# Optimization experiments

Measured on AMD Instinct MI355X. Metric: run time of the kernel, lower is better.

The kernel has to match this reference:

```python
import jax, jax.numpy as jnp
import numpy as np

N_NODES = 100000
N_EDGES = 1600000
D_FEAT = 64
LATENT = 64
N_CLASSES = 16
NEG_SLOPE = 0.01  # flax nn.leaky_relu default negative_slope


def setup_inputs() -> dict:
    key = jax.random.key(0)
    ks = jax.random.split(key, 5)
    nodes = jax.random.normal(ks[0], (N_NODES, D_FEAT), dtype=jnp.float32)
    senders = jax.random.randint(ks[1], (N_EDGES,), 0, N_NODES)
    receivers = jax.random.randint(ks[2], (N_EDGES,), 0, N_NODES)
    # learned params (flax Dense: y = x @ kernel + bias)
    W0 = jax.random.normal(ks[3], (D_FEAT, LATENT), dtype=jnp.float32) / jnp.sqrt(D_FEAT)
    b0 = jnp.zeros((LATENT,), jnp.float32)
    W1 = jax.random.normal(ks[4], (LATENT, N_CLASSES), dtype=jnp.float32) / jnp.sqrt(LATENT)
    b1 = jnp.zeros((N_CLASSES,), jnp.float32)
    return {"nodes": nodes, "senders": senders, "receivers": receivers,
            "W0": W0, "b0": b0, "W1": W1, "b1": b1}


def _gcn_forward(nodes, W0, b0, W1, b1, senders, receivers):
    n = nodes.shape[0]
    ones = jnp.ones_like(senders, dtype=nodes.dtype)
    deg_s = jax.ops.segment_sum(ones, senders, n)    # out-degree of each node as sender
    deg_r = jax.ops.segment_sum(ones, receivers, n)  # in-degree of each node as receiver

    # Layer 1: GraphConvolution(Dense(latent), symmetric_normalization=True)
    h = nodes @ W0 + b0                                                  # [N, latent]
    h = h * jax.lax.rsqrt(jnp.maximum(deg_s, 1.0))[:, None]
    h = jax.ops.segment_sum(h[senders], receivers, n)                    # gather-scatter over edges
    h = h * jax.lax.rsqrt(jnp.maximum(deg_r, 1.0))[:, None]
    h = jnp.where(h >= 0, h, NEG_SLOPE * h)                              # leaky_relu

    # Layer 2: GraphConvolution(Dense(classes)+sigmoid, symmetric_normalization=False)
    z = jax.nn.sigmoid(h @ W1 + b1)                                      # [N, classes]
    out = jax.ops.segment_sum(z[senders], receivers, n)                  # unnormalized aggregation
    return out


def reference(nodes, senders, receivers, W0, b0, W1, b1):
    return _gcn_forward(nodes, W0, b0, W1, b1, senders, receivers)
```

## Files before the change

kernel.cpp:

```cpp
#include <hip/hip_runtime.h>
#include <hip/hip_bf16.h>

#define N_NODES 100000
#define N_EDGES 1600000
#define D 64
#define C 16
#define NEG_SLOPE 0.01f
#define MCAP 64

typedef unsigned int uint32;
typedef unsigned short ushort16;

__device__ __forceinline__ float bf2f(uint32 u) {
    return __uint_as_float(u << 16);
}
__device__ __forceinline__ ushort16 f2bf(float f) {
    __hip_bfloat16 b = __float2bfloat16(f);
    return *reinterpret_cast<ushort16*>(&b);
}

__global__ __launch_bounds__(256) void kA(
        const int* __restrict__ senders, const int* __restrict__ receivers,
        const float* __restrict__ nodes, const float* __restrict__ W0,
        const float* __restrict__ b0,
        int* __restrict__ cnt_s, int* __restrict__ cnt_r,
        int* __restrict__ bucket, ushort16* __restrict__ h) {
    int bid = blockIdx.x;
    if (bid % 5 == 0) {
        int e = (bid / 5) * 256 + threadIdx.x;
        if (e < N_EDGES) {
            int s = senders[e];
            int r = receivers[e];
            atomicAdd(&cnt_s[s], 1);
            int slot = atomicAdd(&cnt_r[r], 1);
            if (slot < MCAP) bucket[r * MCAP + slot] = s;
        }
    } else {
        int gbid = bid - bid / 5 - 1;
        int node = gbid * 4 + (threadIdx.x >> 6);
        int f = threadIdx.x & 63;
        const float* __restrict__ row = nodes + (size_t)node * D;
        float acc = b0[f];
#pragma unroll
        for (int k = 0; k < D; ++k)
            acc = fmaf(row[k], W0[k * D + f], acc);
        h[(size_t)node * D + f] = f2bf(acc);
    }
}

__global__ __launch_bounds__(256) void kB(
        const int* __restrict__ cnt_s, const int* __restrict__ cnt_r,
        const int* __restrict__ bucket, const ushort16* __restrict__ h,
        const float* __restrict__ W1, const float* __restrict__ b1,
        ushort16* __restrict__ z) {
    __shared__ float sm[4][64];
    int wid = threadIdx.x >> 6, lane = threadIdx.x & 63;
    int node = blockIdx.x * 4 + wid;
    int deg = cnt_r[node];
    if (deg > MCAP) deg = MCAP;
    const int* __restrict__ row = bucket + node * MCAP;

    int my = 0; float rq = 0.f;
    if (lane < deg) {
        my = row[lane];
        int ds = cnt_s[my];
        rq = rsqrtf((float)(ds > 1 ? ds : 1));
    }
    int half = lane >> 5, hl = lane & 31;
    float a0 = 0.f, a1 = 0.f;
    for (int k2 = 0; 2 * k2 < deg; ++k2) {
        int ei = 2 * k2 + half;
        int src = __shfl(my, ei, 64);
        float rs = __shfl(rq, ei, 64);
        uint32 w = *(const uint32*)(h + (size_t)src * D + hl * 2);
        if (ei < deg) {
            a0 = fmaf(rs, bf2f(w & 0xffffu), a0);
            a1 = fmaf(rs, bf2f(w >> 16), a1);
        }
    }
    a0 += __shfl_down(a0, 32, 64);
    a1 += __shfl_down(a1, 32, 64);
    if (half == 0) {
        float rr = rsqrtf((float)(deg > 1 ? deg : 1));
        float v0 = a0 * rr; v0 = (v0 >= 0.f) ? v0 : NEG_SLOPE * v0;
        float v1 = a1 * rr; v1 = (v1 >= 0.f) ? v1 : NEG_SLOPE * v1;
        sm[wid][2 * hl] = v0;
        sm[wid][2 * hl + 1] = v1;
    }
    __syncthreads();

    int c = lane & 15, q = lane >> 4;
    float p = 0.f;
#pragma unroll
    for (int i = 0; i < 16; ++i)
        p = fmaf(sm[wid][q * 16 + i], W1[(q * 16 + i) * C + c], p);
    p += __shfl_xor(p, 16, 64);
    p += __shfl_xor(p, 32, 64);
    if (lane < 16) {
        float zc = 1.f / (1.f + expf(-(p + b1[c])));
        z[(size_t)node * C + c] = f2bf(zc);
    }
}

__global__ __launch_bounds__(256) void kC(
        const int* __restrict__ cnt_r, const int* __restrict__ bucket,
        const ushort16* __restrict__ z, float* __restrict__ out) {
    int idx = blockIdx.x * 256 + threadIdx.x;
    int node = idx >> 6;
    int lane = threadIdx.x & 63;
    int g = lane >> 3, p = lane & 7;
    int deg = cnt_r[node];
    if (deg > MCAP) deg = MCAP;
    const int* __restrict__ row = bucket + node * MCAP;

    int my = (lane < deg) ? row[lane] : 0;
    float a0 = 0.f, a1 = 0.f;
    for (int k8 = 0; 8 * k8 < deg; ++k8) {
        int ei = 8 * k8 + g;
        int src = __shfl(my, ei, 64);
        uint32 w = *(const uint32*)(z + (size_t)src * C + p * 2);
        float f0 = bf2f(w & 0xffffu);
        float f1 = bf2f(w >> 16);
        if (ei < deg) { a0 += f0; a1 += f1; }
    }
    a0 += __shfl_xor(a0, 8, 64);  a1 += __shfl_xor(a1, 8, 64);
    a0 += __shfl_xor(a0, 16, 64); a1 += __shfl_xor(a1, 16, 64);
    a0 += __shfl_xor(a0, 32, 64); a1 += __shfl_xor(a1, 32, 64);
    if (lane < 8) {
        float2 o; o.x = a0; o.y = a1;
        *(float2*)(out + (size_t)node * C + p * 2) = o;
    }
}

extern "C" void kernel_launch(void* const* d_in, const int* in_sizes, int n_in,
                              void* d_out, int out_size, void* d_ws, size_t ws_size,
                              hipStream_t stream) {
    const float* nodes     = (const float*)d_in[0];
    const int*   senders   = (const int*)d_in[1];
    const int*   receivers = (const int*)d_in[2];
    const float* W0        = (const float*)d_in[3];
    const float* b0        = (const float*)d_in[4];
    const float* W1        = (const float*)d_in[5];
    const float* b1        = (const float*)d_in[6];
    float* out = (float*)d_out;

    int* cnt_s  = (int*)d_ws;
    int* cnt_r  = cnt_s + N_NODES;
    int* bucket = cnt_r + N_NODES;
    ushort16* h = (ushort16*)(bucket + (size_t)N_NODES * MCAP);
    ushort16* z = h + (size_t)N_NODES * D;

    hipMemsetAsync(cnt_s, 0, 2 * N_NODES * sizeof(int), stream);

    kA<<<31250, 256, 0, stream>>>(senders, receivers, nodes, W0, b0,
                                  cnt_s, cnt_r, bucket, h);

    kB<<<25000, 256, 0, stream>>>(cnt_s, cnt_r, bucket, h, W1, b1, z);

    kC<<<25000, 256, 0, stream>>>(cnt_r, bucket, z, out);
}
```

Baseline: 326.2 us.

## Replace sender-degree atomics with LDS byte histograms and precomputed rsqrt norms

Drops the global atomicAdd on cnt_s. Sender out-degrees are now counted by 512 blocks, each building a packed 8-bit-per-node shared-memory histogram for one node range and edge slice. A new reduction kernel sums these partial histograms and writes rsqrt(deg) per node, so kB loads a precomputed norm instead of computing it. The node GEMM and both gather loops are also widened to 4-element vector loads and accumulators. Risks: 8-bit counters per slice could overflow if one node receives more than 255 sends within a 25000-edge slice, and there is an extra kernel launch and extra traffic for the partial buffers.

```diff
diff --git a/kernel.cpp b/kernel.cpp
--- a/kernel.cpp
+++ b/kernel.cpp
@@ -1,58 +1,122 @@
 #include <hip/hip_runtime.h>
 #include <hip/hip_bf16.h>
 
-#define N_NODES 100000
-#define N_EDGES 1600000
+#define NN 100000
+#define NE 1600000
 #define D 64
 #define C 16
 #define NEG_SLOPE 0.01f
 #define MCAP 64
 
-typedef unsigned int uint32;
-typedef unsigned short ushort16;
-
-__device__ __forceinline__ float bf2f(uint32 u) {
-    return __uint_as_float(u << 16);
-}
-__device__ __forceinline__ ushort16 f2bf(float f) {
+#define NRANGE 8
+#define RW 12544
+#define WPR 3136
+#define NSLICE 64
+#define EPS 25000
+#define B_HIST (NRANGE * NSLICE)
+
+#define B_BUILD 6250
+#define B_GEMM 6250
+
+typedef unsigned int u32;
+typedef unsigned short u16;
+
+__device__ __forceinline__ float bf2f(u32 u) { return __uint_as_float(u << 16); }
+__device__ __forceinline__ u16 f2bf(float f) {
     __hip_bfloat16 b = __float2bfloat16(f);
-    return *reinterpret_cast<ushort16*>(&b);
+    return *reinterpret_cast<u16*>(&b);
 }
 
 __global__ __launch_bounds__(256) void kA(
         const int* __restrict__ senders, const int* __restrict__ receivers,
         const float* __restrict__ nodes, const float* __restrict__ W0,
         const float* __restrict__ b0,
-        int* __restrict__ cnt_s, int* __restrict__ cnt_r,
-        int* __restrict__ bucket, ushort16* __restrict__ h) {
-    int bid = blockIdx.x;
-    if (bid % 5 == 0) {
-        int e = (bid / 5) * 256 + threadIdx.x;
-        if (e < N_EDGES) {
+        int* __restrict__ cnt_r, int* __restrict__ bucket,
+        u16* __restrict__ h, u32* __restrict__ part) {
+    __shared__ u32 smh[WPR];
+    int bid = blockIdx.x, t = threadIdx.x;
+
+    if (bid < 2 * B_BUILD) {
+        if ((bid & 1) == 0) {
+            int e = (bid >> 1) * 256 + t;
             int s = senders[e];
             int r = receivers[e];
-            atomicAdd(&cnt_s[s], 1);
             int slot = atomicAdd(&cnt_r[r], 1);
             if (slot < MCAP) bucket[r * MCAP + slot] = s;
+        } else {
+            int wv = (bid >> 1) * 4 + (t >> 6);
+            int lane = t & 63;
+            int nsub = lane >> 4, q = lane & 15;
+            int node = wv * 4 + nsub;
+            const float* __restrict__ row = nodes + (size_t)node * D;
+            float4 acc = ((const float4*)b0)[q];
+#pragma unroll 16
+            for (int k = 0; k < D; ++k) {
+                float rk = row[k];
+                float4 w4 = ((const float4*)(W0 + k * D))[q];
+                acc.x = fmaf(rk, w4.x, acc.x);
+                acc.y = fmaf(rk, w4.y, acc.y);
+                acc.z = fmaf(rk, w4.z, acc.z);
+                acc.w = fmaf(rk, w4.w, acc.w);
+            }
+            uint2 pk;
+            pk.x = (u32)f2bf(acc.x) | ((u32)f2bf(acc.y) << 16);
+            pk.y = (u32)f2bf(acc.z) | ((u32)f2bf(acc.w) << 16);
+            *(uint2*)(h + (size_t)node * D + q * 4) = pk;
         }
     } else {
-        int gbid = bid - bid / 5 - 1;
-        int node = gbid * 4 + (threadIdx.x >> 6);
-        int f = threadIdx.x & 63;
-        const float* __restrict__ row = nodes + (size_t)node * D;
-        float acc = b0[f];
-#pragma unroll
-        for (int k = 0; k < D; ++k)
-            acc = fmaf(row[k], W0[k * D + f], acc);
-        h[(size_t)node * D + f] = f2bf(acc);
+        int hb = bid - 2 * B_BUILD;
+        int rr = hb & 7, sl = hb >> 3;
+        int lo = rr * RW;
+        for (int i = t; i < WPR; i += 256) smh[i] = 0u;
+        __syncthreads();
+        const int* __restrict__ sp = senders + sl * EPS;
+        for (int i = t; i < EPS; i += 256) {
+            int local = sp[i] - lo;
+            if ((u32)local < (u32)RW)
+                atomicAdd(&smh[local >> 2], 1u << ((local & 3) * 8));
+        }
+        __syncthreads();
+        u32* __restrict__ dst = part + (size_t)hb * WPR;
+        for (int i = t; i < WPR; i += 256) dst[i] = smh[i];
+    }
+}
+
+__global__ __launch_bounds__(256) void k0b(const u32* __restrict__ part,
+                                           float* __restrict__ rnorm_s) {
+    int tid = blockIdx.x * 256 + threadIdx.x;
+    int rr = tid / WPR;
+    int w = tid - rr * WPR;
+    const u32* __restrict__ p = part + (size_t)rr * WPR + w;
+    u32 acc0 = 0, acc1 = 0;
+#pragma unroll 8
+    for (int sl = 0; sl < NSLICE; ++sl) {
+        u32 v = p[(size_t)(sl * 8) * WPR];
+        acc0 += v & 0x00FF00FFu;
+        acc1 += (v >> 8) & 0x00FF00FFu;
+    }
+    int node = rr * RW + w * 4;
+    u32 c0 = acc0 & 0xFFFFu, c1 = acc1 & 0xFFFFu, c2 = acc0 >> 16, c3 = acc1 >> 16;
+    if (node + 3 < NN) {
+        float4 o;
+        o.x = rsqrtf((float)(c0 > 1u ? c0 : 1u));
+        o.y = rsqrtf((float)(c1 > 1u ? c1 : 1u));
+        o.z = rsqrtf((float)(c2 > 1u ? c2 : 1u));
+        o.w = rsqrtf((float)(c3 > 1u ? c3 : 1u));
+        *(float4*)(rnorm_s + node) = o;
+    } else {
+        u32 cc[4] = {c0, c1, c2, c3};
+        for (int k = 0; k < 4; ++k)
+            if (node + k < NN)
+                rnorm_s[node + k] = rsqrtf((float)(cc[k] > 1u ? cc[k] : 1u));
     }
 }
 
 __global__ __launch_bounds__(256) void kB(
-        const int* __restrict__ cnt_s, const int* __restrict__ cnt_r,
-        const int* __restrict__ bucket, const ushort16* __restrict__ h,
+        const int* __restrict__ cnt_r, const int* __restrict__ bucket,
+        const float* __restrict__ rnorm_s, const u16* __restrict__ h,
         const float* __restrict__ W1, const float* __restrict__ b1,
-        ushort16* __restrict__ z) {
+        u16* __restrict__ z) {
     __shared__ float sm[4][64];
     int wid = threadIdx.x >> 6, lane = threadIdx.x & 63;
     int node = blockIdx.x * 4 + wid;
@@ -63,29 +127,36 @@
     int my = 0; float rq = 0.f;
     if (lane < deg) {
         my = row[lane];
-        int ds = cnt_s[my];
-        rq = rsqrtf((float)(ds > 1 ? ds : 1));
-    }
-    int half = lane >> 5, hl = lane & 31;
-    float a0 = 0.f, a1 = 0.f;
-    for (int k2 = 0; 2 * k2 < deg; ++k2) {
-        int ei = 2 * k2 + half;
+        rq = rnorm_s[my];
+    }
+    int qtr = lane >> 4, ql = lane & 15;
+    float a0 = 0.f, a1 = 0.f, a2 = 0.f, a3 = 0.f;
+    for (int j = 0; j < deg; j += 4) {
+        int ei = j + qtr;
         int src = __shfl(my, ei, 64);
         float rs = __shfl(rq, ei, 64);
-        uint32 w = *(const uint32*)(h + (size_t)src * D + hl * 2);
+        uint2 w2 = *(const uint2*)(h + (size_t)src * D + ql * 4);
         if (ei < deg) {
-            a0 = fmaf(rs, bf2f(w & 0xffffu), a0);
-            a1 = fmaf(rs, bf2f(w >> 16), a1);
-        }
-    }
-    a0 += __shfl_down(a0, 32, 64);
-    a1 += __shfl_down(a1, 32, 64);
-    if (half == 0) {
-        float rr = rsqrtf((float)(deg > 1 ? deg : 1));
-        float v0 = a0 * rr; v0 = (v0 >= 0.f) ? v0 : NEG_SLOPE * v0;
-        float v1 = a1 * rr; v1 = (v1 >= 0.f) ? v1 : NEG_SLOPE * v1;
-        sm[wid][2 * hl] = v0;
-        sm[wid][2 * hl + 1] = v1;
+            a0 = fmaf(rs, bf2f(w2.x & 0xffffu), a0);
+            a1 = fmaf(rs, bf2f(w2.x >> 16),     a1);
+            a2 = fmaf(rs, bf2f(w2.y & 0xffffu), a2);
+            a3 = fmaf(rs, bf2f(w2.y >> 16),     a3);
+        }
+    }
+    a0 += __shfl_xor(a0, 16, 64); a0 += __shfl_xor(a0, 32, 64);
+    a1 += __shfl_xor(a1, 16, 64); a1 += __shfl_xor(a1, 32, 64);
+    a2 += __shfl_xor(a2, 16, 64); a2 += __shfl_xor(a2, 32, 64);
+    a3 += __shfl_xor(a3, 16, 64); a3 += __shfl_xor(a3, 32, 64);
+    if (qtr == 0) {
+        float rn = rsqrtf((float)(deg > 1 ? deg : 1));
+        float v0 = a0 * rn; v0 = (v0 >= 0.f) ? v0 : NEG_SLOPE * v0;
+        float v1 = a1 * rn; v1 = (v1 >= 0.f) ? v1 : NEG_SLOPE * v1;
+        float v2 = a2 * rn; v2 = (v2 >= 0.f) ? v2 : NEG_SLOPE * v2;
+        float v3 = a3 * rn; v3 = (v3 >= 0.f) ? v3 : NEG_SLOPE * v3;
+        sm[wid][ql * 4 + 0] = v0;
+        sm[wid][ql * 4 + 1] = v1;
+        sm[wid][ql * 4 + 2] = v2;
+        sm[wid][ql * 4 + 3] = v3;
     }
     __syncthreads();
 
@@ -104,31 +175,39 @@
 
 __global__ __launch_bounds__(256) void kC(
         const int* __restrict__ cnt_r, const int* __restrict__ bucket,
-        const ushort16* __restrict__ z, float* __restrict__ out) {
+        const u16* __restrict__ z, float* __restrict__ out) {
     int idx = blockIdx.x * 256 + threadIdx.x;
     int node = idx >> 6;
     int lane = threadIdx.x & 63;
-    int g = lane >> 3, p = lane & 7;
     int deg = cnt_r[node];
     if (deg > MCAP) deg = MCAP;
     const int* __restrict__ row = bucket + node * MCAP;
 
     int my = (lane < deg) ? row[lane] : 0;
-    float a0 = 0.f, a1 = 0.f;
-    for (int k8 = 0; 8 * k8 < deg; ++k8) {
-        int ei = 8 * k8 + g;
+    int g = lane >> 2, p = lane & 3;
+    float a0 = 0.f, a1 = 0.f, a2 = 0.f, a3 = 0.f;
+    for (int j = 0; j < deg; j += 16) {
+        int ei = j + g;
         int src = __shfl(my, ei, 64);
-        uint32 w = *(const uint32*)(z + (size_t)src * C + p * 2);
-        float f0 = bf2f(w & 0xffffu);
-        float f1 = bf2f(w >> 16);
-        if (ei < deg) { a0 += f0; a1 += f1; }
-    }
-    a0 += __shfl_xor(a0, 8, 64);  a1 += __shfl_xor(a1, 8, 64);
-    a0 += __shfl_xor(a0, 16, 64); a1 += __shfl_xor(a1, 16, 64);
-    a0 += __shfl_xor(a0, 32, 64); a1 += __shfl_xor(a1, 32, 64);
-    if (lane < 8) {
-        float2 o; o.x = a0; o.y = a1;
-        *(float2*)(out + (size_t)node * C + p * 2) = o;
+        uint2 w2 = *(const uint2*)(z + (size_t)src * C + p * 4);
+        if (ei < deg) {
+            a0 += bf2f(w2.x & 0xffffu);
+            a1 += bf2f(w2.x >> 16);
+            a2 += bf2f(w2.y & 0xffffu);
+            a3 += bf2f(w2.y >> 16);
+        }
+    }
+    a0 += __shfl_xor(a0, 4, 64); a0 += __shfl_xor(a0, 8, 64);
+    a0 += __shfl_xor(a0, 16, 64); a0 += __shfl_xor(a0, 32, 64);
+    a1 += __shfl_xor(a1, 4, 64); a1 += __shfl_xor(a1, 8, 64);
+    a1 += __shfl_xor(a1, 16, 64); a1 += __shfl_xor(a1, 32, 64);
+    a2 += __shfl_xor(a2, 4, 64); a2 += __shfl_xor(a2, 8, 64);
+    a2 += __shfl_xor(a2, 16, 64); a2 += __shfl_xor(a2, 32, 64);
+    a3 += __shfl_xor(a3, 4, 64); a3 += __shfl_xor(a3, 8, 64);
+    a3 += __shfl_xor(a3, 16, 64); a3 += __shfl_xor(a3, 32, 64);
+    if (lane < 4) {
+        float4 o; o.x = a0; o.y = a1; o.z = a2; o.w = a3;
+        *(float4*)(out + (size_t)node * C + p * 4) = o;
     }
 }
 
@@ -144,18 +223,19 @@
     const float* b1        = (const float*)d_in[6];
     float* out = (float*)d_out;
 
-    int* cnt_s  = (int*)d_ws;
-    int* cnt_r  = cnt_s + N_NODES;
-    int* bucket = cnt_r + N_NODES;
-    ushort16* h = (ushort16*)(bucket + (size_t)N_NODES * MCAP);
-    ushort16* z = h + (size_t)N_NODES * D;
-
-    hipMemsetAsync(cnt_s, 0, 2 * N_NODES * sizeof(int), stream);
-
-    kA<<<31250, 256, 0, stream>>>(senders, receivers, nodes, W0, b0,
-                                  cnt_s, cnt_r, bucket, h);
-
-    kB<<<25000, 256, 0, stream>>>(cnt_s, cnt_r, bucket, h, W1, b1, z);
-
+    char* wsb = (char*)d_ws;
+    int*   cnt_r   = (int*)wsb;
+    u32*   part    = (u32*)(wsb + 400000);
+    float* rnorm_s = (float*)(wsb + 6822528);
+    int*   bucket  = (int*)(wsb + 7222528);
+    u16*   h       = (u16*)(wsb + 32822528);
+    u16*   z       = (u16*)(wsb + 45622528);
+
+    hipMemsetAsync(cnt_r, 0, NN * sizeof(int), stream);
+
+    kA<<<2 * B_BUILD + B_HIST, 256, 0, stream>>>(senders, receivers, nodes, W0, b0,
+                                                 cnt_r, bucket, h, part);
+    k0b<<<98, 256, 0, stream>>>(part, rnorm_s);
+    kB<<<25000, 256, 0, stream>>>(cnt_r, bucket, rnorm_s, h, W1, b1, z);
     kC<<<25000, 256, 0, stream>>>(cnt_r, bucket, z, out);
 }
```

Measured after the change: 319.4 us. 1.02x faster.
